# Performance work log

Hardware: AMD Instinct MI355X
Metric: run time of the kernel (lower is better)

The kernel has to match this reference:

```python
import jax, jax.numpy as jnp
import numpy as np

BATCH, TOK, DIM, OUT = 4, 2048, 4096, 4096
E, R, TOP_K = 8, 16, 2
SCALING = 16.0 / R  # lora_alpha / r


def setup_inputs() -> dict:
    key = jax.random.key(0)
    ks = jax.random.split(key, 6)
    return {
        "x": jax.random.normal(ks[0], (BATCH, TOK, DIM), dtype=jnp.float32),
        "W_base": jax.random.normal(ks[1], (OUT, DIM), dtype=jnp.float32) / np.sqrt(DIM),
        "b_base": jax.random.normal(ks[2], (OUT,), dtype=jnp.float32) * 0.01,
        "W_gate": jax.random.normal(ks[3], (E, DIM), dtype=jnp.float32) * 0.01,
        "A": jax.random.normal(ks[4], (E, R, DIM), dtype=jnp.float32) / np.sqrt(DIM),
        "B": jax.random.normal(ks[5], (OUT, OUT // OUT * R * 0 + R), dtype=jnp.float32)[None].repeat(E, 0) * 0.0 + jax.random.normal(ks[5], (E, OUT, R), dtype=jnp.float32) * 0.02,
    }


def reference(x, W_base, b_base, W_gate, A, B):
    # Base frozen linear: [B,N,D] @ [D,O] -> [B,N,O]
    result = jnp.einsum("bnd,od->bno", x, W_base) + b_base
    # Gating
    logits = jnp.einsum("bnd,ed->bne", x, W_gate)
    probs = jax.nn.softmax(logits.astype(jnp.float32), axis=-1)  # fp32 softmax
    top_p, top_i = jax.lax.top_k(probs, TOP_K)  # [B,N,K]
    top_p = top_p / jnp.sum(top_p, axis=-1, keepdims=True)  # top_k > 1 branch
    top_p = top_p.astype(x.dtype)
    # Scatter top-k probs back to dense [B,N,E] routing weights
    route_w = jnp.sum(jax.nn.one_hot(top_i, E, dtype=x.dtype) * top_p[..., None], axis=-2)
    # Per-expert LoRA: down-project all tokens for all experts (r is small),
    # weight by routing, then up-project and sum over experts.
    h = jnp.einsum("bnd,erd->bner", x, A)          # [B,N,E,r]
    hw = h * route_w[..., None]                      # mask/combine weighting
    delta = jnp.einsum("bner,eor->bno", hw, B)      # [B,N,O]
    return result + delta * SCALING
```

## Files before the change

### kernel.cpp

```cpp
#include <hip/hip_runtime.h>
#include <hip/hip_bf16.h>
#include <cstdint>

#define TOKENS 8192
#define DIM_   4096
#define OUTD   4096
#define NE     8
#define NR     16
#define LORA_COLS (NE*NR)
#define KCAT  (DIM_ + LORA_COLS)
#define NTILES (KCAT/64)
#define HSPLIT 8
#define HKC    (DIM_/HSPLIT)

typedef __attribute__((ext_vector_type(8))) short short8;
typedef __attribute__((ext_vector_type(4))) float f32x4;

__device__ __forceinline__ unsigned short f2bf(float f) {
  union { float f; unsigned u; } v; v.f = f;
  unsigned r = v.u + 0x7FFFu + ((v.u >> 16) & 1u);
  return (unsigned short)(r >> 16);
}

__device__ __forceinline__ void load_lds16(const void* g, void* l) {
  auto gp = reinterpret_cast<const __attribute__((address_space(1))) unsigned int*>(
      reinterpret_cast<uintptr_t>(g));
  auto lp = reinterpret_cast<__attribute__((address_space(3))) unsigned int*>(
      reinterpret_cast<uintptr_t>(l));
  __builtin_amdgcn_global_load_lds(gp, lp, 16, 0, 0);
}

#define BAR() asm volatile("s_barrier" ::: "memory")
#define LGKM(N) do { asm volatile("s_waitcnt lgkmcnt(" #N ")" ::: "memory"); \
                     __builtin_amdgcn_sched_barrier(0); } while (0)
#define VMW(N) asm volatile("s_waitcnt vmcnt(" #N ")" ::: "memory")

__global__ __launch_bounds__(256) void fused_prep_kernel(
    const float* __restrict__ x, const float* __restrict__ Wg,
    const float* __restrict__ W, const float* __restrict__ Bm,
    const float* __restrict__ Am, unsigned short* __restrict__ Wcat,
    unsigned short* __restrict__ Acat, unsigned short* __restrict__ Xcat,
    int* __restrict__ ridx, float* __restrict__ rw, float scaling) {
  __shared__ float red[32 * 257];
  __shared__ float lg[32];
  int tid = threadIdx.x;
  int bb = blockIdx.x;
  if (bb < OUTD) {
    const float4* src = (const float4*)(W + (size_t)bb * DIM_);
    unsigned short* dst = Wcat + (size_t)bb * KCAT;
#pragma unroll
    for (int j = 0; j < DIM_ / 1024; ++j) {
      float4 v = src[j * 256 + tid];
      ushort4 o; o.x = f2bf(v.x); o.y = f2bf(v.y); o.z = f2bf(v.z); o.w = f2bf(v.w);
      *(ushort4*)(dst + (size_t)(j * 256 + tid) * 4) = o;
    }
    if (tid < LORA_COLS) {
      int e = tid >> 4, r = tid & 15;
      dst[DIM_ + tid] = f2bf(scaling * Bm[((size_t)e * OUTD + bb) * NR + r]);
    }
    return;
  }
  if (bb < OUTD + LORA_COLS) {
    int i = bb - OUTD;
    const float4* src = (const float4*)(Am + (size_t)i * DIM_);
    unsigned short* dst = Acat + (size_t)i * DIM_;
#pragma unroll
    for (int j = 0; j < DIM_ / 1024; ++j) {
      float4 v = src[j * 256 + tid];
      ushort4 o; o.x = f2bf(v.x); o.y = f2bf(v.y); o.z = f2bf(v.z); o.w = f2bf(v.w);
      *(ushort4*)(dst + (size_t)(j * 256 + tid) * 4) = o;
    }
    return;
  }
  int t0 = (bb - OUTD - LORA_COLS) * 4;
  float acc[4][8];
#pragma unroll
  for (int ti = 0; ti < 4; ++ti)
#pragma unroll
    for (int e = 0; e < 8; ++e) acc[ti][e] = 0.f;
  const float4* x4 = (const float4*)x;
  const float4* wg4 = (const float4*)Wg;
#pragma unroll
  for (int j = 0; j < 4; ++j) {
    int dpos = j * 256 + tid;
    float4 wg[8];
#pragma unroll
    for (int e = 0; e < 8; ++e) wg[e] = wg4[e * 1024 + dpos];
#pragma unroll
    for (int ti = 0; ti < 4; ++ti) {
      float4 v = x4[(size_t)(t0 + ti) * 1024 + dpos];
      ushort4 o; o.x = f2bf(v.x); o.y = f2bf(v.y); o.z = f2bf(v.z); o.w = f2bf(v.w);
      *(ushort4*)&Xcat[(size_t)(t0 + ti) * KCAT + (size_t)dpos * 4] = o;
#pragma unroll
      for (int e = 0; e < 8; ++e)
        acc[ti][e] += v.x * wg[e].x + v.y * wg[e].y + v.z * wg[e].z + v.w * wg[e].w;
    }
  }
#pragma unroll
  for (int p = 0; p < 32; ++p) red[p * 257 + tid] = acc[p >> 3][p & 7];
  __syncthreads();
  {
    int p = tid >> 3, part = tid & 7;
    float s = 0.f;
#pragma unroll
    for (int i = 0; i < 32; ++i) s += red[p * 257 + part * 32 + i];
    s += __shfl_xor(s, 1);
    s += __shfl_xor(s, 2);
    s += __shfl_xor(s, 4);
    if (part == 0) lg[p] = s;
  }
  __syncthreads();
  if (tid < 4) {
    float l[8];
#pragma unroll
    for (int e = 0; e < 8; ++e) l[e] = lg[tid * 8 + e];
    int i0 = 0; float m0 = l[0];
#pragma unroll
    for (int e = 1; e < 8; ++e) if (l[e] > m0) { m0 = l[e]; i0 = e; }
    int i1 = -1; float m1 = -3.4e38f;
#pragma unroll
    for (int e = 0; e < 8; ++e) if (e != i0 && l[e] > m1) { m1 = l[e]; i1 = e; }
    float w0 = 1.0f / (1.0f + expf(m1 - m0));
    int t = t0 + tid;
    ridx[t * 2] = i0; ridx[t * 2 + 1] = i1;
    rw[t * 2] = w0;  rw[t * 2 + 1] = 1.0f - w0;
  }
}

template <int MODE>
__global__ __launch_bounds__(256) void gemm_kernel(
    const unsigned short* __restrict__ Aop, const unsigned short* __restrict__ Bop,
    float* __restrict__ Cout, unsigned short* __restrict__ CoutBf,
    const float* __restrict__ bias, const int* __restrict__ ridx,
    const float* __restrict__ rw,
    int M, int N, int K, int lda, int ldb, int ldc) {
  __shared__ __align__(16) unsigned short lsA[128 * 32];
  __shared__ __align__(16) unsigned short lsB[128 * 32];
  int tid = threadIdx.x;
  int lane = tid & 63, wave = tid >> 6;
  int wm = wave >> 1, wn = wave & 1;
  int row0 = blockIdx.x * 128, col0 = blockIdx.y * 128;

  f32x4 acc[4][4];
#pragma unroll
  for (int a = 0; a < 4; ++a)
#pragma unroll
    for (int b = 0; b < 4; ++b) acc[a][b] = (f32x4){0.f, 0.f, 0.f, 0.f};

  int lrow = lane >> 2;
  int lcol = (lane & 3) << 3;
  int fr = lane & 15, fk = (lane >> 4) << 3;

  const unsigned short* gA0 = Aop + (size_t)(row0 + wave * 32 + lrow) * lda + lcol;
  const unsigned short* gA1 = Aop + (size_t)(row0 + wave * 32 + 16 + lrow) * lda + lcol;
  const unsigned short* gB0 = Bop + (size_t)(col0 + wave * 32 + lrow) * ldb + lcol;
  const unsigned short* gB1 = Bop + (size_t)(col0 + wave * 32 + 16 + lrow) * ldb + lcol;

  for (int k0 = 0; k0 < K; k0 += 32) {
    load_lds16(gA0 + k0, lsA + wave * 1024);
    load_lds16(gA1 + k0, lsA + wave * 1024 + 512);
    load_lds16(gB0 + k0, lsB + wave * 1024);
    load_lds16(gB1 + k0, lsB + wave * 1024 + 512);
    __syncthreads();
    short8 af[4], bfr[4];
#pragma unroll
    for (int mi = 0; mi < 4; ++mi)
      af[mi] = *(const short8*)&lsA[(wm * 64 + mi * 16 + fr) * 32 + fk];
#pragma unroll
    for (int ni = 0; ni < 4; ++ni)
      bfr[ni] = *(const short8*)&lsB[(wn * 64 + ni * 16 + fr) * 32 + fk];
#pragma unroll
    for (int mi = 0; mi < 4; ++mi)
#pragma unroll
      for (int ni = 0; ni < 4; ++ni)
        acc[mi][ni] = __builtin_amdgcn_mfma_f32_16x16x32_bf16(af[mi], bfr[ni], acc[mi][ni], 0, 0, 0);
    __syncthreads();
  }

  int fg = lane >> 4;
  if (MODE == 0) {
#pragma unroll
    for (int ni = 0; ni < 4; ++ni) {
      int col = col0 + wn * 64 + ni * 16 + fr;
      float bv = bias[col];
#pragma unroll
      for (int mi = 0; mi < 4; ++mi)
#pragma unroll
        for (int j = 0; j < 4; ++j) {
          int row = row0 + wm * 64 + mi * 16 + fg * 4 + j;
          Cout[(size_t)row * ldc + col] = acc[mi][ni][j] + bv;
        }
    }
  } else {
#pragma unroll
    for (int mi = 0; mi < 4; ++mi)
#pragma unroll
      for (int j = 0; j < 4; ++j) {
        int row = row0 + wm * 64 + mi * 16 + fg * 4 + j;
        int i0 = ridx[row * 2], i1 = ridx[row * 2 + 1];
        float w0 = rw[row * 2], w1 = rw[row * 2 + 1];
#pragma unroll
        for (int ni = 0; ni < 4; ++ni) {
          int col = wn * 64 + ni * 16 + fr;
          int e = col >> 4;
          float w = (e == i0) ? w0 : ((e == i1) ? w1 : 0.f);
          CoutBf[(size_t)row * ldc + col] = f2bf(w * acc[mi][ni][j]);
        }
      }
  }
}

__global__ __launch_bounds__(256) void gemm_h_sk_kernel(
    const unsigned short* __restrict__ Aop,
    const unsigned short* __restrict__ Bop,
    float* __restrict__ Hpart) {
  __shared__ __align__(16) unsigned short lsA[128 * 32];
  __shared__ __align__(16) unsigned short lsB[128 * 32];
  int tid = threadIdx.x;
  int lane = tid & 63, wave = tid >> 6;
  int wm = wave >> 1, wn = wave & 1;
  int row0 = blockIdx.x * 128;
  int s = blockIdx.y;
  int kbeg = s * HKC;

  f32x4 acc[4][4];
#pragma unroll
  for (int a = 0; a < 4; ++a)
#pragma unroll
    for (int b = 0; b < 4; ++b) acc[a][b] = (f32x4){0.f, 0.f, 0.f, 0.f};

  int lrow = lane >> 2;
  int lcol = (lane & 3) << 3;
  int fr = lane & 15, fk = (lane >> 4) << 3;

  const unsigned short* gA0 = Aop + (size_t)(row0 + wave * 32 + lrow) * KCAT + lcol;
  const unsigned short* gA1 = Aop + (size_t)(row0 + wave * 32 + 16 + lrow) * KCAT + lcol;
  const unsigned short* gB0 = Bop + (size_t)(wave * 32 + lrow) * DIM_ + lcol;
  const unsigned short* gB1 = Bop + (size_t)(wave * 32 + 16 + lrow) * DIM_ + lcol;

  for (int k0 = kbeg; k0 < kbeg + HKC; k0 += 32) {
    load_lds16(gA0 + k0, lsA + wave * 1024);
    load_lds16(gA1 + k0, lsA + wave * 1024 + 512);
    load_lds16(gB0 + k0, lsB + wave * 1024);
    load_lds16(gB1 + k0, lsB + wave * 1024 + 512);
    __syncthreads();
    short8 af[4], bfr[4];
#pragma unroll
    for (int mi = 0; mi < 4; ++mi)
      af[mi] = *(const short8*)&lsA[(wm * 64 + mi * 16 + fr) * 32 + fk];
#pragma unroll
    for (int ni = 0; ni < 4; ++ni)
      bfr[ni] = *(const short8*)&lsB[(wn * 64 + ni * 16 + fr) * 32 + fk];
#pragma unroll
    for (int mi = 0; mi < 4; ++mi)
#pragma unroll
      for (int ni = 0; ni < 4; ++ni)
        acc[mi][ni] = __builtin_amdgcn_mfma_f32_16x16x32_bf16(af[mi], bfr[ni], acc[mi][ni], 0, 0, 0);
    __syncthreads();
  }

  int fg = lane >> 4;
  float* outp = Hpart + (size_t)s * TOKENS * 128;
#pragma unroll
  for (int ni = 0; ni < 4; ++ni) {
    int col = wn * 64 + ni * 16 + fr;
#pragma unroll
    for (int mi = 0; mi < 4; ++mi)
#pragma unroll
      for (int j = 0; j < 4; ++j) {
        int row = row0 + wm * 64 + mi * 16 + fg * 4 + j;
        outp[(size_t)row * 128 + col] = acc[mi][ni][j];
      }
  }
}

__global__ __launch_bounds__(256) void h_combine_kernel(
    const float* __restrict__ Hpart, const int* __restrict__ ridx,
    const float* __restrict__ rw, unsigned short* __restrict__ Xcat) {
  int gid = blockIdx.x * 256 + threadIdx.x;
  int t = gid >> 7, c = gid & 127;
  float s = 0.f;
#pragma unroll
  for (int i = 0; i < HSPLIT; ++i) s += Hpart[(size_t)i * TOKENS * 128 + gid];
  int e = c >> 4;
  int i0 = ridx[t * 2], i1 = ridx[t * 2 + 1];
  float w = (e == i0) ? rw[t * 2] : ((e == i1) ? rw[t * 2 + 1] : 0.f);
  Xcat[(size_t)t * KCAT + DIM_ + c] = f2bf(w * s);
}

#define RD_A4(dst, base, ks, mi0) do { \
  dst[0] = *(const short8*)((base) + (((mi0)+0)*2+(ks))*1024); \
  dst[1] = *(const short8*)((base) + (((mi0)+1)*2+(ks))*1024); \
  dst[2] = *(const short8*)((base) + (((mi0)+2)*2+(ks))*1024); \
  dst[3] = *(const short8*)((base) + (((mi0)+3)*2+(ks))*1024); } while (0)
#define RD_B4(dst, base, ks) do { \
  dst[0] = *(const short8*)((base) + 0*2048 + (ks)*1024); \
  dst[1] = *(const short8*)((base) + 1*2048 + (ks)*1024); \
  dst[2] = *(const short8*)((base) + 2*2048 + (ks)*1024); \
  dst[3] = *(const short8*)((base) + 3*2048 + (ks)*1024); } while (0)
#define MFMA_BLK(a4, b4, m0) do { \
  __builtin_amdgcn_s_setprio(1); \
  _Pragma("unroll") \
  for (int mi = 0; mi < 4; ++mi) { \
    _Pragma("unroll") \
    for (int ni = 0; ni < 4; ++ni) { \
      acc[(m0)+mi][ni] = __builtin_amdgcn_mfma_f32_16x16x32_bf16( \
          b4[ni], a4[mi], acc[(m0)+mi][ni], 0, 0, 0); } } \
  __builtin_amdgcn_s_setprio(0); } while (0)
#define STAGE(srcp, kofs, dst) do { \
  load_lds16((srcp) + (kofs), (dst)); \
  load_lds16((srcp) + (kofs) + 32, (dst) + 1024); } while (0)

#define GTILE(RB, SB, KN, DOSTAGE) do { \
  short8 aL[4], aH[4], a1L[4], a1H[4], b0f[4], b1f[4]; \
  if (DOSTAGE) { \
    STAGE(sA0, KN, dA0 + (SB)); STAGE(sA1, KN, dA1 + (SB)); \
    STAGE(sB0, KN, dB0 + (SB)); STAGE(sB1, KN, dB1 + (SB)); \
  } \
  RD_A4(aL, rdA + (RB), 0, 0); RD_B4(b0f, rdB + (RB), 0); \
  RD_A4(aH, rdA + (RB), 0, 4); \
  LGKM(4); \
  MFMA_BLK(aL, b0f, 0); \
  RD_A4(a1L, rdA + (RB), 1, 0); RD_B4(b1f, rdB + (RB), 1); \
  LGKM(8); \
  MFMA_BLK(aH, b0f, 4); \
  RD_A4(a1H, rdA + (RB), 1, 4); \
  LGKM(4); \
  MFMA_BLK(a1L, b1f, 0); \
  LGKM(0); \
  MFMA_BLK(a1H, b1f, 4); \
  if (DOSTAGE) VMW(0); \
  BAR(); \
} while (0)

__global__ __launch_bounds__(512, 2) void gemm256_kernel(
    const unsigned short* __restrict__ Aop,
    const unsigned short* __restrict__ Bop,
    float* __restrict__ Cout, const float* __restrict__ bias) {
  extern __shared__ char lds[];
  const int tid = threadIdx.x;
  const int lane = tid & 63, wave = tid >> 6;
  const int wm = wave >> 2, wn = wave & 3;
  const int fr = lane & 15, kg = lane >> 4;

  const int bid = blockIdx.x;
  const int swz = (bid & 7) * 64 + (bid >> 3);
  const int mt = swz >> 4, nt = swz & 15;
  const int row0 = mt * 256, col0 = nt * 256;

  const int srow = lane >> 2;
  const int scol = ((lane & 3) * 8) ^ (((lane >> 5) & 1) * 16);
  const unsigned short* sA0 = Aop + (size_t)(row0 +       wave * 16 + srow) * KCAT + scol;
  const unsigned short* sA1 = Aop + (size_t)(row0 + 128 + wave * 16 + srow) * KCAT + scol;
  const unsigned short* sB0 = Bop + (size_t)(col0 +       wave * 16 + srow) * KCAT + scol;
  const unsigned short* sB1 = Bop + (size_t)(col0 + 128 + wave * 16 + srow) * KCAT + scol;

  char* dA0 = lds +      0 + wave * 2048;
  char* dA1 = lds +  16384 + wave * 2048;
  char* dB0 = lds +  32768 + wave * 2048;
  char* dB1 = lds +  49152 + wave * 2048;

  const int swzo = (kg * 16) ^ ((fr >> 3) << 5);
  const char* rdA = lds + wm * 16384 + fr * 64 + swzo;
  const char* rdB = lds + 32768 + (wn >> 1) * 16384 + (wn & 1) * 8192 + fr * 64 + swzo;

  f32x4 acc[8][4];
#pragma unroll
  for (int a = 0; a < 8; ++a)
#pragma unroll
    for (int b = 0; b < 4; ++b) acc[a][b] = (f32x4){0.f, 0.f, 0.f, 0.f};

  STAGE(sA0, 0, dA0); STAGE(sA1, 0, dA1);
  STAGE(sB0, 0, dB0); STAGE(sB1, 0, dB1);
  VMW(0);
  BAR();

  for (int i = 0; i < NTILES / 2 - 1; ++i) {
    const int k1 = (2 * i + 1) * 64, k2 = k1 + 64;
    GTILE(0,     65536, k1, true);
    GTILE(65536, 0,     k2, true);
  }
  GTILE(0, 65536, 65 * 64, true);
  GTILE(65536, 0, 0, false);

#pragma unroll
  for (int ni = 0; ni < 4; ++ni) {
    int colb = col0 + wn * 64 + ni * 16 + kg * 4;
    float4 bv = *(const float4*)&bias[colb];
#pragma unroll
    for (int mi = 0; mi < 8; ++mi) {
      int row = row0 + wm * 128 + mi * 16 + fr;
      float4 v;
      v.x = acc[mi][ni][0] + bv.x;
      v.y = acc[mi][ni][1] + bv.y;
      v.z = acc[mi][ni][2] + bv.z;
      v.w = acc[mi][ni][3] + bv.w;
      *(float4*)&Cout[(size_t)row * OUTD + colb] = v;
    }
  }
}

extern "C" void kernel_launch(void* const* d_in, const int* in_sizes, int n_in,
                              void* d_out, int out_size, void* d_ws, size_t ws_size,
                              hipStream_t stream) {
  const float* x  = (const float*)d_in[0];
  const float* Wb = (const float*)d_in[1];
  const float* bb = (const float*)d_in[2];
  const float* Wg = (const float*)d_in[3];
  const float* Am = (const float*)d_in[4];
  const float* Bm = (const float*)d_in[5];
  float* out = (float*)d_out;

  unsigned short* Wcat = (unsigned short*)d_ws;
  unsigned short* Xcat = Wcat + (size_t)OUTD * KCAT;
  unsigned short* Acat = Xcat + (size_t)TOKENS * KCAT;
  int*   ridx = (int*)(Acat + (size_t)LORA_COLS * DIM_);
  float* rw   = (float*)(ridx + (size_t)TOKENS * 2);
  float* Hpart = (float*)(rw + (size_t)TOKENS * 2);

  const size_t ws_needed = (size_t)((char*)(Hpart + (size_t)HSPLIT * TOKENS * 128)
                                    - (char*)d_ws);
  const bool use_splitk = (ws_size >= ws_needed);

  const float scaling = 16.0f / (float)NR;

  hipFuncSetAttribute((const void*)gemm256_kernel,
                      hipFuncAttributeMaxDynamicSharedMemorySize, 131072);

  fused_prep_kernel<<<dim3(OUTD + LORA_COLS + TOKENS / 4), dim3(256), 0, stream>>>(
      x, Wg, Wb, Bm, Am, Wcat, Acat, Xcat, ridx, rw, scaling);
  if (use_splitk) {
    gemm_h_sk_kernel<<<dim3(TOKENS / 128, HSPLIT), dim3(256), 0, stream>>>(
        Xcat, Acat, Hpart);
    h_combine_kernel<<<dim3(TOKENS * 128 / 256), dim3(256), 0, stream>>>(
        Hpart, ridx, rw, Xcat);
  } else {
    gemm_kernel<1><<<dim3(TOKENS / 128, 1), dim3(256), 0, stream>>>(
        Xcat, Acat, (float*)nullptr, Xcat + DIM_, (const float*)nullptr,
        ridx, rw, TOKENS, LORA_COLS, DIM_, KCAT, DIM_, KCAT);
  }
  gemm256_kernel<<<dim3(512), dim3(512), 131072, stream>>>(Xcat, Wcat, out, bb);
}
```

Measured before the change: 325.3 us.

## Load GEMM B operand directly into registers instead of staging through LDS

The main GEMM now stages only the A (activation) tile through LDS. Each wave loads its B (weight) fragments directly from global memory into double-buffered registers, prefetching the next k-tile while computing the current one. This halves the dynamic LDS allocation and removes the LDS writes and reads for B. In exchange, waves sharing a column slice issue duplicate global loads, register pressure rises, and there is a risk of spills or weaker latency hiding.

```diff
diff --git a/kernel.cpp b/kernel.cpp
--- a/kernel.cpp
+++ b/kernel.cpp
@@ -293,44 +293,59 @@
   dst[1] = *(const short8*)((base) + (((mi0)+1)*2+(ks))*1024); \
   dst[2] = *(const short8*)((base) + (((mi0)+2)*2+(ks))*1024); \
   dst[3] = *(const short8*)((base) + (((mi0)+3)*2+(ks))*1024); } while (0)
-#define RD_B4(dst, base, ks) do { \
-  dst[0] = *(const short8*)((base) + 0*2048 + (ks)*1024); \
-  dst[1] = *(const short8*)((base) + 1*2048 + (ks)*1024); \
-  dst[2] = *(const short8*)((base) + 2*2048 + (ks)*1024); \
-  dst[3] = *(const short8*)((base) + 3*2048 + (ks)*1024); } while (0)
-#define MFMA_BLK(a4, b4, m0) do { \
+#define MFMA_BLK(a4, bArr, ks, m0) do { \
   __builtin_amdgcn_s_setprio(1); \
   _Pragma("unroll") \
   for (int mi = 0; mi < 4; ++mi) { \
     _Pragma("unroll") \
     for (int ni = 0; ni < 4; ++ni) { \
       acc[(m0)+mi][ni] = __builtin_amdgcn_mfma_f32_16x16x32_bf16( \
-          b4[ni], a4[mi], acc[(m0)+mi][ni], 0, 0, 0); } } \
+          bArr[ni*2+(ks)], a4[mi], acc[(m0)+mi][ni], 0, 0, 0); } } \
   __builtin_amdgcn_s_setprio(0); } while (0)
-#define STAGE(srcp, kofs, dst) do { \
-  load_lds16((srcp) + (kofs), (dst)); \
-  load_lds16((srcp) + (kofs) + 32, (dst) + 1024); } while (0)
-
-#define GTILE(RB, SB, KN, DOSTAGE) do { \
-  short8 aL[4], aH[4], a1L[4], a1H[4], b0f[4], b1f[4]; \
-  if (DOSTAGE) { \
-    STAGE(sA0, KN, dA0 + (SB)); STAGE(sA1, KN, dA1 + (SB)); \
-    STAGE(sB0, KN, dB0 + (SB)); STAGE(sB1, KN, dB1 + (SB)); \
-  } \
-  RD_A4(aL, rdA + (RB), 0, 0); RD_B4(b0f, rdB + (RB), 0); \
-  RD_A4(aH, rdA + (RB), 0, 4); \
-  LGKM(4); \
-  MFMA_BLK(aL, b0f, 0); \
-  RD_A4(a1L, rdA + (RB), 1, 0); RD_B4(b1f, rdB + (RB), 1); \
-  LGKM(8); \
-  MFMA_BLK(aH, b0f, 4); \
+#define STAGEA(KN, SB) do { \
+  load_lds16(sA0 + (KN), dA0 + (SB)); \
+  load_lds16(sA0 + (KN) + 32, dA0 + (SB) + 1024); \
+  load_lds16(sA1 + (KN), dA1 + (SB)); \
+  load_lds16(sA1 + (KN) + 32, dA1 + (SB) + 1024); } while (0)
+#define LOADB(dst, KN) do { \
+  _Pragma("unroll") \
+  for (int ni = 0; ni < 4; ++ni) { \
+    dst[ni*2+0] = *(const short8*)(gBp + (size_t)ni * 16 * KCAT + (KN)); \
+    dst[ni*2+1] = *(const short8*)(gBp + (size_t)ni * 16 * KCAT + (KN) + 32); \
+  } } while (0)
+
+#define GTILE_FULL(RB, SB, KN, bCur, bNxt) do { \
+  STAGEA(KN, SB); \
+  LOADB(bNxt, KN); \
+  short8 aL[4], aH[4], a1L[4], a1H[4]; \
+  RD_A4(aL, rdA + (RB), 0, 0); RD_A4(aH, rdA + (RB), 0, 4); \
+  LGKM(4); \
+  MFMA_BLK(aL, bCur, 0, 0); \
+  RD_A4(a1L, rdA + (RB), 1, 0); \
+  LGKM(4); \
+  MFMA_BLK(aH, bCur, 0, 4); \
   RD_A4(a1H, rdA + (RB), 1, 4); \
   LGKM(4); \
-  MFMA_BLK(a1L, b1f, 0); \
+  MFMA_BLK(a1L, bCur, 1, 0); \
   LGKM(0); \
-  MFMA_BLK(a1H, b1f, 4); \
-  if (DOSTAGE) VMW(0); \
+  MFMA_BLK(a1H, bCur, 1, 4); \
+  VMW(8); \
   BAR(); \
+} while (0)
+
+#define GTILE_LAST(RB, bCur) do { \
+  short8 aL[4], aH[4], a1L[4], a1H[4]; \
+  RD_A4(aL, rdA + (RB), 0, 0); RD_A4(aH, rdA + (RB), 0, 4); \
+  LGKM(4); \
+  MFMA_BLK(aL, bCur, 0, 0); \
+  RD_A4(a1L, rdA + (RB), 1, 0); \
+  LGKM(4); \
+  MFMA_BLK(aH, bCur, 0, 4); \
+  RD_A4(a1H, rdA + (RB), 1, 4); \
+  LGKM(4); \
+  MFMA_BLK(a1L, bCur, 1, 0); \
+  LGKM(0); \
+  MFMA_BLK(a1H, bCur, 1, 4); \
 } while (0)
 
 __global__ __launch_bounds__(512, 2) void gemm256_kernel(
@@ -352,17 +367,14 @@
   const int scol = ((lane & 3) * 8) ^ (((lane >> 5) & 1) * 16);
   const unsigned short* sA0 = Aop + (size_t)(row0 +       wave * 16 + srow) * KCAT + scol;
   const unsigned short* sA1 = Aop + (size_t)(row0 + 128 + wave * 16 + srow) * KCAT + scol;
-  const unsigned short* sB0 = Bop + (size_t)(col0 +       wave * 16 + srow) * KCAT + scol;
-  const unsigned short* sB1 = Bop + (size_t)(col0 + 128 + wave * 16 + srow) * KCAT + scol;
-
-  char* dA0 = lds +      0 + wave * 2048;
-  char* dA1 = lds +  16384 + wave * 2048;
-  char* dB0 = lds +  32768 + wave * 2048;
-  char* dB1 = lds +  49152 + wave * 2048;
+
+  const unsigned short* gBp = Bop + (size_t)(col0 + wn * 64 + fr) * KCAT + kg * 8;
+
+  char* dA0 = lds +     0 + wave * 2048;
+  char* dA1 = lds + 16384 + wave * 2048;
 
   const int swzo = (kg * 16) ^ ((fr >> 3) << 5);
   const char* rdA = lds + wm * 16384 + fr * 64 + swzo;
-  const char* rdB = lds + 32768 + (wn >> 1) * 16384 + (wn & 1) * 8192 + fr * 64 + swzo;
 
   f32x4 acc[8][4];
 #pragma unroll
@@ -370,18 +382,20 @@
 #pragma unroll
     for (int b = 0; b < 4; ++b) acc[a][b] = (f32x4){0.f, 0.f, 0.f, 0.f};
 
-  STAGE(sA0, 0, dA0); STAGE(sA1, 0, dA1);
-  STAGE(sB0, 0, dB0); STAGE(sB1, 0, dB1);
-  VMW(0);
+  short8 bA[8], bB[8];
+
+  STAGEA(0, 0);
+  LOADB(bA, 0);
+  VMW(8);
   BAR();
 
   for (int i = 0; i < NTILES / 2 - 1; ++i) {
     const int k1 = (2 * i + 1) * 64, k2 = k1 + 64;
-    GTILE(0,     65536, k1, true);
-    GTILE(65536, 0,     k2, true);
-  }
-  GTILE(0, 65536, 65 * 64, true);
-  GTILE(65536, 0, 0, false);
+    GTILE_FULL(0,     32768, k1, bA, bB);
+    GTILE_FULL(32768, 0,     k2, bB, bA);
+  }
+  GTILE_FULL(0, 32768, 65 * 64, bA, bB);
+  GTILE_LAST(32768, bB);
 
 #pragma unroll
   for (int ni = 0; ni < 4; ++ni) {
@@ -425,7 +439,7 @@
   const float scaling = 16.0f / (float)NR;
 
   hipFuncSetAttribute((const void*)gemm256_kernel,
-                      hipFuncAttributeMaxDynamicSharedMemorySize, 131072);
+                      hipFuncAttributeMaxDynamicSharedMemorySize, 65536);
 
   fused_prep_kernel<<<dim3(OUTD + LORA_COLS + TOKENS / 4), dim3(256), 0, stream>>>(
       x, Wg, Wb, Bm, Am, Wcat, Acat, Xcat, ridx, rw, scaling);
@@ -439,5 +453,5 @@
         Xcat, Acat, (float*)nullptr, Xcat + DIM_, (const float*)nullptr,
         ridx, rw, TOKENS, LORA_COLS, DIM_, KCAT, DIM_, KCAT);
   }
-  gemm256_kernel<<<dim3(512), dim3(512), 131072, stream>>>(Xcat, Wcat, out, bb);
-}
+  gemm256_kernel<<<dim3(512), dim3(512), 65536, stream>>>(Xcat, Wcat, out, bb);
+}
```

Measured after the change: 450.0 us. 38.3% more time.

## Switch main GEMM from 16x16x32 to 32x32x16 bf16 MFMA tiles

Applied to the files above, without the earlier changes.

Replaces the 16x16x32 MFMA instructions in the 256x256 GEMM with 32x32x16 ones, giving each wave a 4x2 grid of 32x32 accumulators. It rewrites the LDS fragment read addressing, the K-step schedule (four k-steps of 16 with double-buffered fragments) and the output epilogue to match the new accumulator layout. The aim is fewer LDS fragment reads per MFMA FLOP and higher MFMA throughput per instruction. The new lane-to-LDS mapping must agree exactly with the existing swizzled staging layout, which risks bank conflicts or wrong results.

```diff
diff --git a/kernel.cpp b/kernel.cpp
--- a/kernel.cpp
+++ b/kernel.cpp
@@ -15,6 +15,7 @@
 
 typedef __attribute__((ext_vector_type(8))) short short8;
 typedef __attribute__((ext_vector_type(4))) float f32x4;
+typedef __attribute__((ext_vector_type(16))) float f32x16;
 
 __device__ __forceinline__ unsigned short f2bf(float f) {
   union { float f; unsigned u; } v; v.f = f;
@@ -288,47 +289,47 @@
   Xcat[(size_t)t * KCAT + DIM_ + c] = f2bf(w * s);
 }
 
-#define RD_A4(dst, base, ks, mi0) do { \
-  dst[0] = *(const short8*)((base) + (((mi0)+0)*2+(ks))*1024); \
-  dst[1] = *(const short8*)((base) + (((mi0)+1)*2+(ks))*1024); \
-  dst[2] = *(const short8*)((base) + (((mi0)+2)*2+(ks))*1024); \
-  dst[3] = *(const short8*)((base) + (((mi0)+3)*2+(ks))*1024); } while (0)
-#define RD_B4(dst, base, ks) do { \
-  dst[0] = *(const short8*)((base) + 0*2048 + (ks)*1024); \
-  dst[1] = *(const short8*)((base) + 1*2048 + (ks)*1024); \
-  dst[2] = *(const short8*)((base) + 2*2048 + (ks)*1024); \
-  dst[3] = *(const short8*)((base) + 3*2048 + (ks)*1024); } while (0)
-#define MFMA_BLK(a4, b4, m0) do { \
+#define RD6(aX, bX, RB, ks) do { \
+  const char* _ab = ((ks) & 1) ? rdAo : rdAe; \
+  const char* _bb = ((ks) & 1) ? rdBo : rdBe; \
+  aX[0] = *(const short8*)(_ab + (RB) + 0 * 4096 + ((ks) >> 1) * 1024); \
+  aX[1] = *(const short8*)(_ab + (RB) + 1 * 4096 + ((ks) >> 1) * 1024); \
+  aX[2] = *(const short8*)(_ab + (RB) + 2 * 4096 + ((ks) >> 1) * 1024); \
+  aX[3] = *(const short8*)(_ab + (RB) + 3 * 4096 + ((ks) >> 1) * 1024); \
+  bX[0] = *(const short8*)(_bb + (RB) + 0 * 4096 + ((ks) >> 1) * 1024); \
+  bX[1] = *(const short8*)(_bb + (RB) + 1 * 4096 + ((ks) >> 1) * 1024); \
+} while (0)
+#define MFMA8(aX, bX) do { \
   __builtin_amdgcn_s_setprio(1); \
   _Pragma("unroll") \
-  for (int mi = 0; mi < 4; ++mi) { \
+  for (int tm = 0; tm < 4; ++tm) { \
     _Pragma("unroll") \
-    for (int ni = 0; ni < 4; ++ni) { \
-      acc[(m0)+mi][ni] = __builtin_amdgcn_mfma_f32_16x16x32_bf16( \
-          b4[ni], a4[mi], acc[(m0)+mi][ni], 0, 0, 0); } } \
+    for (int tn = 0; tn < 2; ++tn) { \
+      acc[tm][tn] = __builtin_amdgcn_mfma_f32_32x32x16_bf16( \
+          bX[tn], aX[tm], acc[tm][tn], 0, 0, 0); } } \
   __builtin_amdgcn_s_setprio(0); } while (0)
 #define STAGE(srcp, kofs, dst) do { \
   load_lds16((srcp) + (kofs), (dst)); \
   load_lds16((srcp) + (kofs) + 32, (dst) + 1024); } while (0)
 
 #define GTILE(RB, SB, KN, DOSTAGE) do { \
-  short8 aL[4], aH[4], a1L[4], a1H[4], b0f[4], b1f[4]; \
+  short8 aP[4], bP[2], aQ[4], bQ[2]; \
   if (DOSTAGE) { \
     STAGE(sA0, KN, dA0 + (SB)); STAGE(sA1, KN, dA1 + (SB)); \
     STAGE(sB0, KN, dB0 + (SB)); STAGE(sB1, KN, dB1 + (SB)); \
   } \
-  RD_A4(aL, rdA + (RB), 0, 0); RD_B4(b0f, rdB + (RB), 0); \
-  RD_A4(aH, rdA + (RB), 0, 4); \
-  LGKM(4); \
-  MFMA_BLK(aL, b0f, 0); \
-  RD_A4(a1L, rdA + (RB), 1, 0); RD_B4(b1f, rdB + (RB), 1); \
-  LGKM(8); \
-  MFMA_BLK(aH, b0f, 4); \
-  RD_A4(a1H, rdA + (RB), 1, 4); \
-  LGKM(4); \
-  MFMA_BLK(a1L, b1f, 0); \
+  RD6(aP, bP, RB, 0); \
+  RD6(aQ, bQ, RB, 1); \
+  LGKM(6); \
+  MFMA8(aP, bP); \
+  RD6(aP, bP, RB, 2); \
+  LGKM(6); \
+  MFMA8(aQ, bQ); \
+  RD6(aQ, bQ, RB, 3); \
+  LGKM(6); \
+  MFMA8(aP, bP); \
   LGKM(0); \
-  MFMA_BLK(a1H, b1f, 4); \
+  MFMA8(aQ, bQ); \
   if (DOSTAGE) VMW(0); \
   BAR(); \
 } while (0)
@@ -341,7 +342,6 @@
   const int tid = threadIdx.x;
   const int lane = tid & 63, wave = tid >> 6;
   const int wm = wave >> 2, wn = wave & 3;
-  const int fr = lane & 15, kg = lane >> 4;
 
   const int bid = blockIdx.x;
   const int swz = (bid & 7) * 64 + (bid >> 3);
@@ -360,15 +360,23 @@
   char* dB0 = lds +  32768 + wave * 2048;
   char* dB1 = lds +  49152 + wave * 2048;
 
-  const int swzo = (kg * 16) ^ ((fr >> 3) << 5);
-  const char* rdA = lds + wm * 16384 + fr * 64 + swzo;
-  const char* rdB = lds + 32768 + (wn >> 1) * 16384 + (wn & 1) * 8192 + fr * 64 + swzo;
-
-  f32x4 acc[8][4];
-#pragma unroll
-  for (int a = 0; a < 8; ++a)
-#pragma unroll
-    for (int b = 0; b < 4; ++b) acc[a][b] = (f32x4){0.f, 0.f, 0.f, 0.f};
+  const int fr16 = lane & 15;
+  const int fr16hi = (lane >> 4) & 1;
+  const int khalf = (lane >> 5) & 1;
+  const int fr8 = (lane >> 3) & 1;
+  const int laneoff = fr16 * 64 + fr16hi * 2048 + khalf * 16 + fr8 * 32;
+  const char* rdAe = lds + wm * 16384 + laneoff;
+  const char* rdAo = lds + wm * 16384 + (laneoff ^ 32);
+  const char* rdBe = lds + 32768 + wn * 8192 + laneoff;
+  const char* rdBo = lds + 32768 + wn * 8192 + (laneoff ^ 32);
+
+  f32x16 acc[4][2];
+#pragma unroll
+  for (int a = 0; a < 4; ++a)
+#pragma unroll
+    for (int b = 0; b < 2; ++b)
+#pragma unroll
+      for (int q = 0; q < 16; ++q) acc[a][b][q] = 0.f;
 
   STAGE(sA0, 0, dA0); STAGE(sA1, 0, dA1);
   STAGE(sB0, 0, dB0); STAGE(sB1, 0, dB1);
@@ -384,18 +392,22 @@
   GTILE(65536, 0, 0, false);
 
 #pragma unroll
-  for (int ni = 0; ni < 4; ++ni) {
-    int colb = col0 + wn * 64 + ni * 16 + kg * 4;
-    float4 bv = *(const float4*)&bias[colb];
-#pragma unroll
-    for (int mi = 0; mi < 8; ++mi) {
-      int row = row0 + wm * 128 + mi * 16 + fr;
-      float4 v;
-      v.x = acc[mi][ni][0] + bv.x;
-      v.y = acc[mi][ni][1] + bv.y;
-      v.z = acc[mi][ni][2] + bv.z;
-      v.w = acc[mi][ni][3] + bv.w;
-      *(float4*)&Cout[(size_t)row * OUTD + colb] = v;
+  for (int tn = 0; tn < 2; ++tn) {
+#pragma unroll
+    for (int tm = 0; tm < 4; ++tm) {
+      int row = row0 + wm * 128 + tm * 32 + (lane & 31);
+      float* outrow = Cout + (size_t)row * OUTD;
+#pragma unroll
+      for (int g = 0; g < 4; ++g) {
+        int col = col0 + wn * 64 + tn * 32 + g * 8 + khalf * 4;
+        float4 bv = *(const float4*)&bias[col];
+        float4 v;
+        v.x = acc[tm][tn][g * 4 + 0] + bv.x;
+        v.y = acc[tm][tn][g * 4 + 1] + bv.y;
+        v.z = acc[tm][tn][g * 4 + 2] + bv.z;
+        v.w = acc[tm][tn][g * 4 + 3] + bv.w;
+        *(float4*)&outrow[col] = v;
+      }
     }
   }
 }
```

Result: slower. 359.2 us (+10.4%).

## Restructure main GEMM tile into barrier-synchronized quadrants; store split-K partials as bf16

Applied to the files above, without the earlier changes.

The 256x256 GEMM inner tile now runs as four quadrant phases. Each phase loads a smaller set of A/B fragments from LDS and issues MFMAs over both k-halves, with s_barrier pairs around each MFMA block so the waves execute in lockstep, ping-pong style. This is meant to overlap LDS reads with MFMA issue across waves and to lower register pressure, at the cost of more barriers and of reloading the A fragments twice per tile. Separately, the split-K LoRA down-projection partials are now written and read as bf16 instead of fp32, which halves that traffic but adds rounding to each partial sum.

```diff
diff --git a/kernel.cpp b/kernel.cpp
--- a/kernel.cpp
+++ b/kernel.cpp
@@ -21,6 +21,9 @@
   unsigned r = v.u + 0x7FFFu + ((v.u >> 16) & 1u);
   return (unsigned short)(r >> 16);
 }
+__device__ __forceinline__ float bf2f(unsigned short u) {
+  union { unsigned u; float f; } v; v.u = ((unsigned)u) << 16; return v.f;
+}
 
 __device__ __forceinline__ void load_lds16(const void* g, void* l) {
   auto gp = reinterpret_cast<const __attribute__((address_space(1))) unsigned int*>(
@@ -33,6 +36,7 @@
 #define BAR() asm volatile("s_barrier" ::: "memory")
 #define LGKM(N) do { asm volatile("s_waitcnt lgkmcnt(" #N ")" ::: "memory"); \
                      __builtin_amdgcn_sched_barrier(0); } while (0)
+#define LGKMW(N) asm volatile("s_waitcnt lgkmcnt(" #N ")" ::: "memory")
 #define VMW(N) asm volatile("s_waitcnt vmcnt(" #N ")" ::: "memory")
 
 __global__ __launch_bounds__(256) void fused_prep_kernel(
@@ -213,7 +217,7 @@
 __global__ __launch_bounds__(256) void gemm_h_sk_kernel(
     const unsigned short* __restrict__ Aop,
     const unsigned short* __restrict__ Bop,
-    float* __restrict__ Hpart) {
+    unsigned short* __restrict__ Hpart) {
   __shared__ __align__(16) unsigned short lsA[128 * 32];
   __shared__ __align__(16) unsigned short lsB[128 * 32];
   int tid = threadIdx.x;
@@ -260,7 +264,7 @@
   }
 
   int fg = lane >> 4;
-  float* outp = Hpart + (size_t)s * TOKENS * 128;
+  unsigned short* outp = Hpart + (size_t)s * TOKENS * 128;
 #pragma unroll
   for (int ni = 0; ni < 4; ++ni) {
     int col = wn * 64 + ni * 16 + fr;
@@ -269,67 +273,79 @@
 #pragma unroll
       for (int j = 0; j < 4; ++j) {
         int row = row0 + wm * 64 + mi * 16 + fg * 4 + j;
-        outp[(size_t)row * 128 + col] = acc[mi][ni][j];
+        outp[(size_t)row * 128 + col] = f2bf(acc[mi][ni][j]);
       }
   }
 }
 
 __global__ __launch_bounds__(256) void h_combine_kernel(
-    const float* __restrict__ Hpart, const int* __restrict__ ridx,
+    const unsigned short* __restrict__ Hpart, const int* __restrict__ ridx,
     const float* __restrict__ rw, unsigned short* __restrict__ Xcat) {
   int gid = blockIdx.x * 256 + threadIdx.x;
   int t = gid >> 7, c = gid & 127;
   float s = 0.f;
 #pragma unroll
-  for (int i = 0; i < HSPLIT; ++i) s += Hpart[(size_t)i * TOKENS * 128 + gid];
+  for (int i = 0; i < HSPLIT; ++i) s += bf2f(Hpart[(size_t)i * TOKENS * 128 + gid]);
   int e = c >> 4;
   int i0 = ridx[t * 2], i1 = ridx[t * 2 + 1];
   float w = (e == i0) ? rw[t * 2] : ((e == i1) ? rw[t * 2 + 1] : 0.f);
   Xcat[(size_t)t * KCAT + DIM_ + c] = f2bf(w * s);
 }
 
-#define RD_A4(dst, base, ks, mi0) do { \
+#define RDA4K(dst, base, ks, mi0) do { \
   dst[0] = *(const short8*)((base) + (((mi0)+0)*2+(ks))*1024); \
   dst[1] = *(const short8*)((base) + (((mi0)+1)*2+(ks))*1024); \
   dst[2] = *(const short8*)((base) + (((mi0)+2)*2+(ks))*1024); \
   dst[3] = *(const short8*)((base) + (((mi0)+3)*2+(ks))*1024); } while (0)
-#define RD_B4(dst, base, ks) do { \
-  dst[0] = *(const short8*)((base) + 0*2048 + (ks)*1024); \
-  dst[1] = *(const short8*)((base) + 1*2048 + (ks)*1024); \
-  dst[2] = *(const short8*)((base) + 2*2048 + (ks)*1024); \
-  dst[3] = *(const short8*)((base) + 3*2048 + (ks)*1024); } while (0)
-#define MFMA_BLK(a4, b4, m0) do { \
+#define RDB1(RB, ni, ks) (*(const short8*)(rdB0 + (RB) + (ni)*2048 + (ks)*1024))
+#define MFMAQ(a0v, a1v, b0v, b1v, m0, n0) do { \
   __builtin_amdgcn_s_setprio(1); \
   _Pragma("unroll") \
   for (int mi = 0; mi < 4; ++mi) { \
     _Pragma("unroll") \
-    for (int ni = 0; ni < 4; ++ni) { \
-      acc[(m0)+mi][ni] = __builtin_amdgcn_mfma_f32_16x16x32_bf16( \
-          b4[ni], a4[mi], acc[(m0)+mi][ni], 0, 0, 0); } } \
+    for (int ni = 0; ni < 2; ++ni) { \
+      acc[(m0)+mi][(n0)+ni] = __builtin_amdgcn_mfma_f32_16x16x32_bf16( \
+          b0v[ni], a0v[mi], acc[(m0)+mi][(n0)+ni], 0, 0, 0); \
+      acc[(m0)+mi][(n0)+ni] = __builtin_amdgcn_mfma_f32_16x16x32_bf16( \
+          b1v[ni], a1v[mi], acc[(m0)+mi][(n0)+ni], 0, 0, 0); } } \
   __builtin_amdgcn_s_setprio(0); } while (0)
 #define STAGE(srcp, kofs, dst) do { \
   load_lds16((srcp) + (kofs), (dst)); \
   load_lds16((srcp) + (kofs) + 32, (dst) + 1024); } while (0)
 
-#define GTILE(RB, SB, KN, DOSTAGE) do { \
-  short8 aL[4], aH[4], a1L[4], a1H[4], b0f[4], b1f[4]; \
+#define QTILE(RB, SB, KN, DOSTAGE) do { \
+  short8 a0v[4], a1v[4], bl0[2], bl1[2], bh0[2], bh1[2]; \
+   \
+  RDA4K(a0v, rdA0 + (RB), 0, 0); \
+  RDA4K(a1v, rdA0 + (RB), 1, 0); \
+  bl0[0] = RDB1(RB, 0, 0); bl0[1] = RDB1(RB, 1, 0); \
+  bl1[0] = RDB1(RB, 0, 1); bl1[1] = RDB1(RB, 1, 1); \
   if (DOSTAGE) { \
     STAGE(sA0, KN, dA0 + (SB)); STAGE(sA1, KN, dA1 + (SB)); \
     STAGE(sB0, KN, dB0 + (SB)); STAGE(sB1, KN, dB1 + (SB)); \
   } \
-  RD_A4(aL, rdA + (RB), 0, 0); RD_B4(b0f, rdB + (RB), 0); \
-  RD_A4(aH, rdA + (RB), 0, 4); \
-  LGKM(4); \
-  MFMA_BLK(aL, b0f, 0); \
-  RD_A4(a1L, rdA + (RB), 1, 0); RD_B4(b1f, rdB + (RB), 1); \
-  LGKM(8); \
-  MFMA_BLK(aH, b0f, 4); \
-  RD_A4(a1H, rdA + (RB), 1, 4); \
-  LGKM(4); \
-  MFMA_BLK(a1L, b1f, 0); \
-  LGKM(0); \
-  MFMA_BLK(a1H, b1f, 4); \
+  LGKMW(8); \
+  BAR(); LGKM(0); \
+  MFMAQ(a0v, a1v, bl0, bl1, 0, 0); \
+  BAR(); \
+   \
+  RDA4K(a0v, rdA0 + (RB), 0, 4); \
+  RDA4K(a1v, rdA0 + (RB), 1, 4); \
+  BAR(); LGKM(0); \
+  MFMAQ(a0v, a1v, bl0, bl1, 4, 0); \
+  BAR(); \
+   \
+  bh0[0] = RDB1(RB, 2, 0); bh0[1] = RDB1(RB, 3, 0); \
+  bh1[0] = RDB1(RB, 2, 1); bh1[1] = RDB1(RB, 3, 1); \
+  BAR(); LGKM(0); \
+  MFMAQ(a0v, a1v, bh0, bh1, 4, 2); \
+  BAR(); \
+   \
+  RDA4K(a0v, rdA0 + (RB), 0, 0); \
+  RDA4K(a1v, rdA0 + (RB), 1, 0); \
   if (DOSTAGE) VMW(0); \
+  BAR(); LGKM(0); \
+  MFMAQ(a0v, a1v, bh0, bh1, 0, 2); \
   BAR(); \
 } while (0)
 
@@ -361,8 +377,8 @@
   char* dB1 = lds +  49152 + wave * 2048;
 
   const int swzo = (kg * 16) ^ ((fr >> 3) << 5);
-  const char* rdA = lds + wm * 16384 + fr * 64 + swzo;
-  const char* rdB = lds + 32768 + (wn >> 1) * 16384 + (wn & 1) * 8192 + fr * 64 + swzo;
+  const char* rdA0 = lds + wm * 16384 + fr * 64 + swzo;
+  const char* rdB0 = lds + 32768 + (wn >> 1) * 16384 + (wn & 1) * 8192 + fr * 64 + swzo;
 
   f32x4 acc[8][4];
 #pragma unroll
@@ -376,12 +392,11 @@
   BAR();
 
   for (int i = 0; i < NTILES / 2 - 1; ++i) {
-    const int k1 = (2 * i + 1) * 64, k2 = k1 + 64;
-    GTILE(0,     65536, k1, true);
-    GTILE(65536, 0,     k2, true);
-  }
-  GTILE(0, 65536, 65 * 64, true);
-  GTILE(65536, 0, 0, false);
+    QTILE(0,     65536, (2 * i + 1) * 64, true);
+    QTILE(65536, 0,     (2 * i + 2) * 64, true);
+  }
+  QTILE(0, 65536, 65 * 64, true);
+  QTILE(65536, 0, 0, false);
 
 #pragma unroll
   for (int ni = 0; ni < 4; ++ni) {
@@ -416,7 +431,7 @@
   unsigned short* Acat = Xcat + (size_t)TOKENS * KCAT;
   int*   ridx = (int*)(Acat + (size_t)LORA_COLS * DIM_);
   float* rw   = (float*)(ridx + (size_t)TOKENS * 2);
-  float* Hpart = (float*)(rw + (size_t)TOKENS * 2);
+  unsigned short* Hpart = (unsigned short*)(rw + (size_t)TOKENS * 2);
 
   const size_t ws_needed = (size_t)((char*)(Hpart + (size_t)HSPLIT * TOKENS * 128)
                                     - (char*)d_ws);
```

After: 354.9 us. 9.1% more time.
